# Kernel optimization log

Measured on AMD Instinct MI355X. Metric: run time of the kernel, lower is better.

Reference implementation:

```python
import jax, jax.numpy as jnp
import numpy as np

B, S, D = 2, 1024, 128


def setup_inputs() -> dict:
    key = jax.random.key(0)
    k1, k2, k3 = jax.random.split(key, 3)
    node_features = jax.random.normal(k1, (B, S, D), dtype=jnp.float32)
    # Linear(2D -> D) then Linear(D -> 1); weights stored as (in, out)
    W1 = jax.random.normal(k2, (2 * D, D), dtype=jnp.float32) * (1.0 / np.sqrt(2 * D))
    b1 = jnp.zeros((D,), dtype=jnp.float32)
    W2 = jax.random.normal(k3, (D, 1), dtype=jnp.float32) * (1.0 / np.sqrt(D))
    b2 = jnp.zeros((1,), dtype=jnp.float32)
    return {"node_features": node_features, "W1": W1, "b1": b1, "W2": W2, "b2": b2}


def reference(node_features, W1, b1, W2, b2):
    # Faithful to: concat(node_i, node_j) @ W1 + b1 -> relu -> @ W2 + b2.
    # Since concat([xi, xj]) @ W1 == xi @ W1[:D] + xj @ W1[D:], project nodes
    # once (O(S*D^2)) and broadcast-add per pair instead of materializing the
    # (B,S,S,2D) concatenated tensor.
    d = node_features.shape[-1]
    hi = node_features @ W1[:d]   # (B,S,D) contribution of node_i
    hj = node_features @ W1[d:]   # (B,S,D) contribution of node_j
    h = jax.nn.relu(hi[:, :, None, :] + hj[:, None, :, :] + b1)  # (B,S,S,D)
    edge_logits = jnp.einsum('bijd,d->bij', h, W2[:, 0]) + b2[0]  # (B,S,S)
    return edge_logits
```

## Files before the change

kernel.cpp:

```cpp
#include <hip/hip_runtime.h>

#define BB 2
#define SDIM 1024
#define DDIM 128
#define K1_ROWS 4

#define F4GET(v,k) ((k)==0?(v).x:((k)==1?(v).y:((k)==2?(v).z:(v).w)))

typedef _Float16 h2v __attribute__((ext_vector_type(2)));
typedef _Float16 h8v __attribute__((ext_vector_type(8)));

__device__ __forceinline__ h2v habs2(h2v t) {
    unsigned u = __builtin_bit_cast(unsigned, t) & 0x7FFF7FFFu;
    return __builtin_bit_cast(h2v, u);
}

__device__ __forceinline__ float hdot2(h2v a, h2v b, float acc) {
#if __has_builtin(__builtin_amdgcn_fdot2)
    return __builtin_amdgcn_fdot2(a, b, acc, false);
#else
    acc = fmaf((float)a.x, (float)b.x, acc);
    return fmaf((float)a.y, (float)b.y, acc);
#endif
}

__global__ __launch_bounds__(256) void proj_kernel(
    const float* __restrict__ x, const float* __restrict__ W1,
    const float* __restrict__ b1, const float* __restrict__ W2,
    const float* __restrict__ b2,
    ushort* __restrict__ hi16, ushort* __restrict__ hjb16,
    float* __restrict__ si2, float* __restrict__ sj2)
{
    __shared__ float sX[K1_ROWS][DDIM];
    __shared__ float sRed[4][K1_ROWS];
    const int tid  = threadIdx.x;
    const int d    = tid & 127;
    const int half = tid >> 7;
    const int r0   = blockIdx.x * K1_ROWS;

    if (tid < K1_ROWS * DDIM / 4) {
        reinterpret_cast<float4*>(&sX[0][0])[tid] =
            reinterpret_cast<const float4*>(x + (size_t)r0 * DDIM)[tid];
    }
    __syncthreads();

    const float* Wh = W1 + (size_t)half * DDIM * DDIM;

    float acc[K1_ROWS];
    #pragma unroll
    for (int r = 0; r < K1_ROWS; ++r) acc[r] = 0.f;

    #pragma unroll 4
    for (int k = 0; k < DDIM; k += 4) {
        float4 xv[K1_ROWS];
        #pragma unroll
        for (int r = 0; r < K1_ROWS; ++r)
            xv[r] = *reinterpret_cast<const float4*>(&sX[r][k]);
        #pragma unroll
        for (int kk = 0; kk < 4; ++kk) {
            float w = Wh[(size_t)(k + kk) * DDIM + d];
            #pragma unroll
            for (int r = 0; r < K1_ROWS; ++r)
                acc[r] = fmaf(F4GET(xv[r], kk), w, acc[r]);
        }
    }

    if (half) {
        const float bv = b1[d];
        #pragma unroll
        for (int r = 0; r < K1_ROWS; ++r) acc[r] += bv;
    }

    ushort* hout = half ? hjb16 : hi16;
    #pragma unroll
    for (int r = 0; r < K1_ROWS; ++r) {
        _Float16 hv = (_Float16)acc[r];
        hout[(size_t)(r0 + r) * DDIM + d] = __builtin_bit_cast(ushort, hv);
    }

    const float wv = W2[d];
    const int lane = tid & 63;
    const int wave = tid >> 6;
    #pragma unroll
    for (int r = 0; r < K1_ROWS; ++r) {
        float v = acc[r] * wv;
        #pragma unroll
        for (int off = 32; off >= 1; off >>= 1)
            v += __shfl_xor(v, off, 64);
        if (lane == 0) sRed[wave][r] = v;
    }
    __syncthreads();
    if (tid < K1_ROWS) {
        si2[r0 + tid] = 0.5f * (sRed[0][tid] + sRed[1][tid]);
    } else if (tid < 2 * K1_ROWS) {
        int r = tid - K1_ROWS;
        sj2[r0 + r] = 0.5f * (sRed[2][r] + sRed[3][r]) + b2[0];
    }
}

__global__ __launch_bounds__(256) void edge_kernel(
    const ushort* __restrict__ hi16, const ushort* __restrict__ hjb16,
    const float* __restrict__ si2, const float* __restrict__ sj2,
    const float* __restrict__ W2, float* __restrict__ out)
{
    __shared__ ushort sHi[64 * DDIM];
    __shared__ ushort sHj[64 * DDIM];
    __shared__ ushort sWh[DDIM];
    __shared__ float  sSi[64];
    __shared__ float  sSj[64];

    const int b   = blockIdx.z;
    const int i0  = blockIdx.y * 64;
    const int j0  = blockIdx.x * 64;
    const int tid = threadIdx.x;

    {
        const h8v* srcI = reinterpret_cast<const h8v*>(hi16  + ((size_t)b * SDIM + i0) * DDIM);
        const h8v* srcJ = reinterpret_cast<const h8v*>(hjb16 + ((size_t)b * SDIM + j0) * DDIM);
        h8v* dI = reinterpret_cast<h8v*>(sHi);
        h8v* dJ = reinterpret_cast<h8v*>(sHj);
        #pragma unroll
        for (int p = 0; p < 4; ++p) {
            int idx = p * 256 + tid;
            int row = idx >> 4, ch = idx & 15;
            dI[row * 16 + (ch ^ (row & 7))]        = srcI[idx];
            dJ[row * 16 + (ch ^ ((row >> 2) & 7))] = srcJ[idx];
        }
    }
    if (tid < DDIM) {
        _Float16 wv = (_Float16)(0.5f * W2[tid]);
        sWh[tid] = __builtin_bit_cast(ushort, wv);
    } else if (tid < DDIM + 64) {
        sSi[tid - DDIM] = si2[b * SDIM + i0 + (tid - DDIM)];
    } else {
        sSj[tid - DDIM - 64] = sj2[b * SDIM + j0 + (tid - DDIM - 64)];
    }
    __syncthreads();

    const int tx = tid & 15;
    const int ty = tid >> 4;
    const int ri = ty * 4;
    const int cj = tx * 4;
    const int bswz = tx & 7;

    float acc[4][4];
    #pragma unroll
    for (int r = 0; r < 4; ++r)
        #pragma unroll
        for (int c = 0; c < 4; ++c) acc[r][c] = 0.f;

    const h8v* sAi = reinterpret_cast<const h8v*>(sHi);
    const h8v* sBj = reinterpret_cast<const h8v*>(sHj);
    const h8v* sWv = reinterpret_cast<const h8v*>(sWh);

    #pragma unroll 2
    for (int ch = 0; ch < 16; ++ch) {
        h8v A[4], Bv[4];
        #pragma unroll
        for (int r = 0; r < 4; ++r)
            A[r] = sAi[(ri + r) * 16 + (ch ^ ((ri + r) & 7))];
        #pragma unroll
        for (int c = 0; c < 4; ++c)
            Bv[c] = sBj[(cj + c) * 16 + (ch ^ bswz)];
        const h8v Wv = sWv[ch];

        #pragma unroll
        for (int r = 0; r < 4; ++r) {
            const h2v* ap = reinterpret_cast<const h2v*>(&A[r]);
            #pragma unroll
            for (int c = 0; c < 4; ++c) {
                const h2v* bp = reinterpret_cast<const h2v*>(&Bv[c]);
                const h2v* wp = reinterpret_cast<const h2v*>(&Wv);
                float a = acc[r][c];
                #pragma unroll
                for (int k = 0; k < 4; ++k) {
                    h2v t = ap[k] + bp[k];
                    a = hdot2(habs2(t), wp[k], a);
                }
                acc[r][c] = a;
            }
        }
    }

    #pragma unroll
    for (int r = 0; r < 4; ++r) {
        const float sv = sSi[ri + r];
        float4 o;
        o.x = acc[r][0] + sv + sSj[cj + 0];
        o.y = acc[r][1] + sv + sSj[cj + 1];
        o.z = acc[r][2] + sv + sSj[cj + 2];
        o.w = acc[r][3] + sv + sSj[cj + 3];
        size_t base = (size_t)b * SDIM * SDIM + (size_t)(i0 + ri + r) * SDIM + j0 + cj;
        *reinterpret_cast<float4*>(out + base) = o;
    }
}

extern "C" void kernel_launch(void* const* d_in, const int* in_sizes, int n_in,
                              void* d_out, int out_size, void* d_ws, size_t ws_size,
                              hipStream_t stream) {
    const float* x  = (const float*)d_in[0];
    const float* W1 = (const float*)d_in[1];
    const float* b1 = (const float*)d_in[2];
    const float* W2 = (const float*)d_in[3];
    const float* b2 = (const float*)d_in[4];
    float* out = (float*)d_out;

    char* ws = (char*)d_ws;
    ushort* hi16  = (ushort*)ws;
    ushort* hjb16 = hi16 + (size_t)BB * SDIM * DDIM;
    float*  si2   = (float*)(hjb16 + (size_t)BB * SDIM * DDIM);
    float*  sj2   = si2 + (size_t)BB * SDIM;

    proj_kernel<<<BB * SDIM / K1_ROWS, 256, 0, stream>>>(x, W1, b1, W2, b2, hi16, hjb16, si2, sj2);
    edge_kernel<<<dim3(SDIM / 64, SDIM / 64, BB), 256, 0, stream>>>(hi16, hjb16, si2, sj2, W2, out);
}
```

Baseline: 28.13 us.

## Split edge kernel D-reduction across two thread groups and halve projection rows

The edge kernel now runs 512 threads per block. Each half computes the same 64x64 output tile over half of the 16 feature chunks, and the two partial sums are combined through shared memory before the store. The LDS swizzle is unified into an XOR of low and high row bits for both tiles. The projection kernel processes 2 rows per block instead of 4, doubling the grid. This adds latency-hiding parallelism in the compute-bound edge loop at the cost of an extra barrier and a shared-memory reduction step.

```diff
diff --git a/kernel.cpp b/kernel.cpp
--- a/kernel.cpp
+++ b/kernel.cpp
@@ -3,7 +3,7 @@
 #define BB 2
 #define SDIM 1024
 #define DDIM 128
-#define K1_ROWS 4
+#define K1_ROWS 2
 
 #define F4GET(v,k) ((k)==0?(v).x:((k)==1?(v).y:((k)==2?(v).z:(v).w)))
 
@@ -22,6 +22,10 @@
     acc = fmaf((float)a.x, (float)b.x, acc);
     return fmaf((float)a.y, (float)b.y, acc);
 #endif
+}
+
+__device__ __forceinline__ int rswz(int row) {
+    return (row & 7) ^ ((row >> 3) & 7);
 }
 
 __global__ __launch_bounds__(256) void proj_kernel(
@@ -98,14 +102,14 @@
     }
 }
 
-__global__ __launch_bounds__(256) void edge_kernel(
+__global__ __launch_bounds__(512) void edge_kernel(
     const ushort* __restrict__ hi16, const ushort* __restrict__ hjb16,
     const float* __restrict__ si2, const float* __restrict__ sj2,
     const float* __restrict__ W2, float* __restrict__ out)
 {
-    __shared__ ushort sHi[64 * DDIM];
-    __shared__ ushort sHj[64 * DDIM];
-    __shared__ ushort sWh[DDIM];
+    __shared__ float4 sTileI[1024];
+    __shared__ float4 sTileJ[1024];
+    __shared__ float4 sWf[16];
     __shared__ float  sSi[64];
     __shared__ float  sSj[64];
 
@@ -117,31 +121,39 @@
     {
         const h8v* srcI = reinterpret_cast<const h8v*>(hi16  + ((size_t)b * SDIM + i0) * DDIM);
         const h8v* srcJ = reinterpret_cast<const h8v*>(hjb16 + ((size_t)b * SDIM + j0) * DDIM);
-        h8v* dI = reinterpret_cast<h8v*>(sHi);
-        h8v* dJ = reinterpret_cast<h8v*>(sHj);
-        #pragma unroll
-        for (int p = 0; p < 4; ++p) {
-            int idx = p * 256 + tid;
+        h8v* dI = reinterpret_cast<h8v*>(sTileI);
+        h8v* dJ = reinterpret_cast<h8v*>(sTileJ);
+        #pragma unroll
+        for (int p = 0; p < 2; ++p) {
+            int idx = p * 512 + tid;
             int row = idx >> 4, ch = idx & 15;
-            dI[row * 16 + (ch ^ (row & 7))]        = srcI[idx];
-            dJ[row * 16 + (ch ^ ((row >> 2) & 7))] = srcJ[idx];
+            int cs  = ch ^ rswz(row);
+            dI[row * 16 + cs] = srcI[idx];
+            dJ[row * 16 + cs] = srcJ[idx];
         }
     }
     if (tid < DDIM) {
         _Float16 wv = (_Float16)(0.5f * W2[tid]);
-        sWh[tid] = __builtin_bit_cast(ushort, wv);
+        reinterpret_cast<ushort*>(sWf)[tid] = __builtin_bit_cast(ushort, wv);
     } else if (tid < DDIM + 64) {
         sSi[tid - DDIM] = si2[b * SDIM + i0 + (tid - DDIM)];
-    } else {
+    } else if (tid < DDIM + 128) {
         sSj[tid - DDIM - 64] = sj2[b * SDIM + j0 + (tid - DDIM - 64)];
     }
     __syncthreads();
 
-    const int tx = tid & 15;
-    const int ty = tid >> 4;
+    const int t8 = tid & 255;
+    const int g  = tid >> 8;
+    const int tx = t8 & 15;
+    const int ty = t8 >> 4;
     const int ri = ty * 4;
     const int cj = tx * 4;
-    const int bswz = tx & 7;
+
+    int swzA[4], swzB[4];
+    #pragma unroll
+    for (int r = 0; r < 4; ++r) swzA[r] = rswz(ri + r);
+    #pragma unroll
+    for (int c = 0; c < 4; ++c) swzB[c] = rswz(cj + c);
 
     float acc[4][4];
     #pragma unroll
@@ -149,19 +161,20 @@
         #pragma unroll
         for (int c = 0; c < 4; ++c) acc[r][c] = 0.f;
 
-    const h8v* sAi = reinterpret_cast<const h8v*>(sHi);
-    const h8v* sBj = reinterpret_cast<const h8v*>(sHj);
-    const h8v* sWv = reinterpret_cast<const h8v*>(sWh);
-
+    const h8v* sAi = reinterpret_cast<const h8v*>(sTileI);
+    const h8v* sBj = reinterpret_cast<const h8v*>(sTileJ);
+    const h8v* sWv = reinterpret_cast<const h8v*>(sWf);
+
+    const int ch0 = g * 8;
     #pragma unroll 2
-    for (int ch = 0; ch < 16; ++ch) {
+    for (int ch = ch0; ch < ch0 + 8; ++ch) {
         h8v A[4], Bv[4];
         #pragma unroll
         for (int r = 0; r < 4; ++r)
-            A[r] = sAi[(ri + r) * 16 + (ch ^ ((ri + r) & 7))];
+            A[r] = sAi[(ri + r) * 16 + (ch ^ swzA[r])];
         #pragma unroll
         for (int c = 0; c < 4; ++c)
-            Bv[c] = sBj[(cj + c) * 16 + (ch ^ bswz)];
+            Bv[c] = sBj[(cj + c) * 16 + (ch ^ swzB[c])];
         const h8v Wv = sWv[ch];
 
         #pragma unroll
@@ -182,16 +195,28 @@
         }
     }
 
-    #pragma unroll
-    for (int r = 0; r < 4; ++r) {
-        const float sv = sSi[ri + r];
-        float4 o;
-        o.x = acc[r][0] + sv + sSj[cj + 0];
-        o.y = acc[r][1] + sv + sSj[cj + 1];
-        o.z = acc[r][2] + sv + sSj[cj + 2];
-        o.w = acc[r][3] + sv + sSj[cj + 3];
-        size_t base = (size_t)b * SDIM * SDIM + (size_t)(i0 + ri + r) * SDIM + j0 + cj;
-        *reinterpret_cast<float4*>(out + base) = o;
+    __syncthreads();
+    if (g == 1) {
+        #pragma unroll
+        for (int r = 0; r < 4; ++r)
+            sTileI[t8 * 4 + (r ^ (t8 & 3))] =
+                make_float4(acc[r][0], acc[r][1], acc[r][2], acc[r][3]);
+    }
+    __syncthreads();
+    if (g == 0) {
+        #pragma unroll
+        for (int r = 0; r < 4; ++r) {
+            const float4 p = sTileI[t8 * 4 + (r ^ (t8 & 3))];
+            const float sv = sSi[ri + r];
+            float4 o;
+            o.x = acc[r][0] + p.x + sv + sSj[cj + 0];
+            o.y = acc[r][1] + p.y + sv + sSj[cj + 1];
+            o.z = acc[r][2] + p.z + sv + sSj[cj + 2];
+            o.w = acc[r][3] + p.w + sv + sSj[cj + 3];
+            size_t base = (size_t)b * SDIM * SDIM
+                        + (size_t)(i0 + ri + r) * SDIM + j0 + cj;
+            *reinterpret_cast<float4*>(out + base) = o;
+        }
     }
 }
 
@@ -212,5 +237,5 @@
     float*  sj2   = si2 + (size_t)BB * SDIM;
 
     proj_kernel<<<BB * SDIM / K1_ROWS, 256, 0, stream>>>(x, W1, b1, W2, b2, hi16, hjb16, si2, sj2);
-    edge_kernel<<<dim3(SDIM / 64, SDIM / 64, BB), 256, 0, stream>>>(hi16, hjb16, si2, sj2, W2, out);
-}
+    edge_kernel<<<dim3(SDIM / 64, SDIM / 64, BB), 512, 0, stream>>>(hi16, hjb16, si2, sj2, W2, out);
+}
```

After: 28.38 us. Within noise of the previous version (+0.9%).

## Replace LDS-tiled edge kernel with register-resident per-lane j rows and broadcast i rows

Applied to the files above, without the earlier changes.

The edge kernel drops shared-memory tiling. Each lane keeps its own 128-wide fp16 hj row and the halved W2 vector in registers, then loops over 8 i rows that every lane of the wave reads from global memory as a broadcast. W2 is converted to fp16 once in the projection kernel, and that kernel's row count per block is halved to launch more blocks. This removes the LDS staging and barriers, but it needs many more VGPRs (about 48 h8v vectors) and gives far less reuse per loaded element, since each output costs the full 128-wide work without register blocking over i.

```diff
diff --git a/kernel.cpp b/kernel.cpp
--- a/kernel.cpp
+++ b/kernel.cpp
@@ -3,7 +3,8 @@
 #define BB 2
 #define SDIM 1024
 #define DDIM 128
-#define K1_ROWS 4
+#define K1_ROWS 2
+#define II 8
 
 #define F4GET(v,k) ((k)==0?(v).x:((k)==1?(v).y:((k)==2?(v).z:(v).w)))
 
@@ -29,7 +30,8 @@
     const float* __restrict__ b1, const float* __restrict__ W2,
     const float* __restrict__ b2,
     ushort* __restrict__ hi16, ushort* __restrict__ hjb16,
-    float* __restrict__ si2, float* __restrict__ sj2)
+    float* __restrict__ si2, float* __restrict__ sj2,
+    ushort* __restrict__ w2h16)
 {
     __shared__ float sX[K1_ROWS][DDIM];
     __shared__ float sRed[4][K1_ROWS];
@@ -79,6 +81,10 @@
     }
 
     const float wv = W2[d];
+    if (!half && blockIdx.x == 0) {
+        _Float16 wh = (_Float16)(0.5f * wv);
+        w2h16[d] = __builtin_bit_cast(ushort, wh);
+    }
     const int lane = tid & 63;
     const int wave = tid >> 6;
     #pragma unroll
@@ -101,97 +107,57 @@
 __global__ __launch_bounds__(256) void edge_kernel(
     const ushort* __restrict__ hi16, const ushort* __restrict__ hjb16,
     const float* __restrict__ si2, const float* __restrict__ sj2,
-    const float* __restrict__ W2, float* __restrict__ out)
+    const ushort* __restrict__ w2h16, float* __restrict__ out)
 {
-    __shared__ ushort sHi[64 * DDIM];
-    __shared__ ushort sHj[64 * DDIM];
-    __shared__ ushort sWh[DDIM];
-    __shared__ float  sSi[64];
-    __shared__ float  sSj[64];
+    const int tid  = threadIdx.x;
+    const int lane = tid & 63;
+    const int wid  = blockIdx.x * 4 + (tid >> 6);
+    const int jg   = wid & 15;
+    const int ig   = (wid >> 4) & 127;
+    const int b    = wid >> 11;
+    const int j    = (jg << 6) + lane;
+    const int i0   = ig * II;
+    const int rowb = b << 10;
 
-    const int b   = blockIdx.z;
-    const int i0  = blockIdx.y * 64;
-    const int j0  = blockIdx.x * 64;
-    const int tid = threadIdx.x;
+    h8v Bv[16];
+    {
+        const h8v* bp = reinterpret_cast<const h8v*>(hjb16 + (size_t)(rowb + j) * DDIM);
+        #pragma unroll
+        for (int ch = 0; ch < 16; ++ch) Bv[ch] = bp[ch];
+    }
+    h8v Wv[16];
+    {
+        const h8v* wp = reinterpret_cast<const h8v*>(w2h16);
+        #pragma unroll
+        for (int ch = 0; ch < 16; ++ch) Wv[ch] = wp[ch];
+    }
+    const float sjv = sj2[rowb + j];
 
-    {
-        const h8v* srcI = reinterpret_cast<const h8v*>(hi16  + ((size_t)b * SDIM + i0) * DDIM);
-        const h8v* srcJ = reinterpret_cast<const h8v*>(hjb16 + ((size_t)b * SDIM + j0) * DDIM);
-        h8v* dI = reinterpret_cast<h8v*>(sHi);
-        h8v* dJ = reinterpret_cast<h8v*>(sHj);
+    #pragma unroll 1
+    for (int ii = 0; ii < II; ++ii) {
+        const int i = i0 + ii;
+        const h8v* hp = reinterpret_cast<const h8v*>(hi16 + (size_t)(rowb + i) * DDIM);
+        h8v H[16];
         #pragma unroll
-        for (int p = 0; p < 4; ++p) {
-            int idx = p * 256 + tid;
-            int row = idx >> 4, ch = idx & 15;
-            dI[row * 16 + (ch ^ (row & 7))]        = srcI[idx];
-            dJ[row * 16 + (ch ^ ((row >> 2) & 7))] = srcJ[idx];
+        for (int ch = 0; ch < 16; ++ch) H[ch] = hp[ch];
+
+        float a0 = 0.f, a1 = 0.f, a2 = 0.f, a3 = 0.f;
+        #pragma unroll
+        for (int ch = 0; ch < 16; ++ch) {
+            const h2v* bp2 = reinterpret_cast<const h2v*>(&Bv[ch]);
+            const h2v* hp2 = reinterpret_cast<const h2v*>(&H[ch]);
+            const h2v* wp2 = reinterpret_cast<const h2v*>(&Wv[ch]);
+            h2v t0 = bp2[0] + hp2[0];
+            h2v t1 = bp2[1] + hp2[1];
+            h2v t2 = bp2[2] + hp2[2];
+            h2v t3 = bp2[3] + hp2[3];
+            a0 = hdot2(habs2(t0), wp2[0], a0);
+            a1 = hdot2(habs2(t1), wp2[1], a1);
+            a2 = hdot2(habs2(t2), wp2[2], a2);
+            a3 = hdot2(habs2(t3), wp2[3], a3);
         }
-    }
-    if (tid < DDIM) {
-        _Float16 wv = (_Float16)(0.5f * W2[tid]);
-        sWh[tid] = __builtin_bit_cast(ushort, wv);
-    } else if (tid < DDIM + 64) {
-        sSi[tid - DDIM] = si2[b * SDIM + i0 + (tid - DDIM)];
-    } else {
-        sSj[tid - DDIM - 64] = sj2[b * SDIM + j0 + (tid - DDIM - 64)];
-    }
-    __syncthreads();
-
-    const int tx = tid & 15;
-    const int ty = tid >> 4;
-    const int ri = ty * 4;
-    const int cj = tx * 4;
-    const int bswz = tx & 7;
-
-    float acc[4][4];
-    #pragma unroll
-    for (int r = 0; r < 4; ++r)
-        #pragma unroll
-        for (int c = 0; c < 4; ++c) acc[r][c] = 0.f;
-
-    const h8v* sAi = reinterpret_cast<const h8v*>(sHi);
-    const h8v* sBj = reinterpret_cast<const h8v*>(sHj);
-    const h8v* sWv = reinterpret_cast<const h8v*>(sWh);
-
-    #pragma unroll 2
-    for (int ch = 0; ch < 16; ++ch) {
-        h8v A[4], Bv[4];
-        #pragma unroll
-        for (int r = 0; r < 4; ++r)
-            A[r] = sAi[(ri + r) * 16 + (ch ^ ((ri + r) & 7))];
-        #pragma unroll
-        for (int c = 0; c < 4; ++c)
-            Bv[c] = sBj[(cj + c) * 16 + (ch ^ bswz)];
-        const h8v Wv = sWv[ch];
-
-        #pragma unroll
-        for (int r = 0; r < 4; ++r) {
-            const h2v* ap = reinterpret_cast<const h2v*>(&A[r]);
-            #pragma unroll
-            for (int c = 0; c < 4; ++c) {
-                const h2v* bp = reinterpret_cast<const h2v*>(&Bv[c]);
-                const h2v* wp = reinterpret_cast<const h2v*>(&Wv);
-                float a = acc[r][c];
-                #pragma unroll
-                for (int k = 0; k < 4; ++k) {
-                    h2v t = ap[k] + bp[k];
-                    a = hdot2(habs2(t), wp[k], a);
-                }
-                acc[r][c] = a;
-            }
-        }
-    }
-
-    #pragma unroll
-    for (int r = 0; r < 4; ++r) {
-        const float sv = sSi[ri + r];
-        float4 o;
-        o.x = acc[r][0] + sv + sSj[cj + 0];
-        o.y = acc[r][1] + sv + sSj[cj + 1];
-        o.z = acc[r][2] + sv + sSj[cj + 2];
-        o.w = acc[r][3] + sv + sSj[cj + 3];
-        size_t base = (size_t)b * SDIM * SDIM + (size_t)(i0 + ri + r) * SDIM + j0 + cj;
-        *reinterpret_cast<float4*>(out + base) = o;
+        const float res = ((a0 + a1) + (a2 + a3)) + si2[rowb + i] + sjv;
+        out[((size_t)(rowb + i) << 10) + j] = res;
     }
 }
 
@@ -206,11 +172,13 @@
     float* out = (float*)d_out;
 
     char* ws = (char*)d_ws;
-    ushort* hi16  = (ushort*)ws;
-    ushort* hjb16 = hi16 + (size_t)BB * SDIM * DDIM;
-    float*  si2   = (float*)(hjb16 + (size_t)BB * SDIM * DDIM);
-    float*  sj2   = si2 + (size_t)BB * SDIM;
+    ushort* hi16   = (ushort*)ws;
+    ushort* hjb16  = hi16 + (size_t)BB * SDIM * DDIM;
+    float*  si2    = (float*)(hjb16 + (size_t)BB * SDIM * DDIM);
+    float*  sj2    = si2 + (size_t)BB * SDIM;
+    ushort* w2h16  = (ushort*)(sj2 + (size_t)BB * SDIM);
 
-    proj_kernel<<<BB * SDIM / K1_ROWS, 256, 0, stream>>>(x, W1, b1, W2, b2, hi16, hjb16, si2, sj2);
-    edge_kernel<<<dim3(SDIM / 64, SDIM / 64, BB), 256, 0, stream>>>(hi16, hjb16, si2, sj2, W2, out);
+    proj_kernel<<<BB * SDIM / K1_ROWS, 256, 0, stream>>>(x, W1, b1, W2, b2,
+                                                         hi16, hjb16, si2, sj2, w2h16);
+    edge_kernel<<<SDIM / 64 * (SDIM / II) * BB / 4, 256, 0, stream>>>(hi16, hjb16, si2, sj2, w2h16, out);
 }
```

After: 37.19 us. +32.2%, slower.
